# Performance work log

Measured on AMD Instinct MI355X. Metric: run time of the kernel, lower is better.

## Reference

```python
import jax, jax.numpy as jnp
import numpy as np

B, T, ENC_H, DEC_H, ATTN = 128, 2048, 512, 512, 128


def setup_inputs() -> dict:
    key = jax.random.key(0)
    k1, k2, k3, k4, k5 = jax.random.split(key, 5)
    s = lambda fan_in: 1.0 / np.sqrt(fan_in)
    return {
        "encoder_outputs": jax.random.normal(k1, (B, T, ENC_H), dtype=jnp.float32),
        "decoder_hidden": jax.random.normal(k2, (B, DEC_H), dtype=jnp.float32),
        # nn.Linear weights are [out_features, in_features]
        "W_enc": jax.random.uniform(k3, (ATTN, ENC_H), jnp.float32, -s(ENC_H), s(ENC_H)),
        "W_dec": jax.random.uniform(k4, (ATTN, DEC_H), jnp.float32, -s(DEC_H), s(DEC_H)),
        "v_w": jax.random.uniform(k5, (1, ATTN), jnp.float32, -s(ATTN), s(ATTN)),
    }


def reference(encoder_outputs, decoder_hidden, W_enc, W_dec, v_w):
    # enc_proj: [B, T, A]
    enc_proj = jnp.einsum("bth,ah->bta", encoder_outputs, W_enc)
    # dec_proj: [B, 1, A]
    dec_proj = jnp.einsum("bh,ah->ba", decoder_hidden, W_dec)[:, None, :]
    energy = jnp.tanh(enc_proj + dec_proj)                      # [B, T, A]
    scores = jnp.einsum("bta,a->bt", energy, v_w[0])            # [B, T]
    weights = jax.nn.softmax(scores, axis=-1)                   # [B, T]
    context = jnp.einsum("bt,bth->bh", weights, encoder_outputs)  # [B, ENC_H]
    return context, weights
```

## Files before the change

kernel.cpp:

```cpp
#include <hip/hip_runtime.h>
#include <hip/hip_bf16.h>

#define B_SZ   128
#define T_SZ   2048
#define ENCH   512
#define ATTN_  128
#define NBLK   256
#define SEGS_PER_BLK 4

typedef __attribute__((ext_vector_type(8))) short short8;
typedef __attribute__((ext_vector_type(4))) float f32x4;

__device__ __forceinline__ unsigned short f2bf_rne(float f) {
  unsigned u = __builtin_bit_cast(unsigned, f);
  u += 0x7FFFu + ((u >> 16) & 1u);
  return (unsigned short)(u >> 16);
}
__device__ __forceinline__ float fast_tanh(float x) {
  float e = __expf(2.f * x);
  return 1.f - __fdividef(2.f, e + 1.f);
}
__device__ __forceinline__ short8 pack8(float4 a, float4 b) {
  union { unsigned u[4]; short8 s; } r;
  asm("v_cvt_pk_bf16_f32 %0, %1, %2" : "=v"(r.u[0]) : "v"(a.x), "v"(a.y));
  asm("v_cvt_pk_bf16_f32 %0, %1, %2" : "=v"(r.u[1]) : "v"(a.z), "v"(a.w));
  asm("v_cvt_pk_bf16_f32 %0, %1, %2" : "=v"(r.u[2]) : "v"(b.x), "v"(b.y));
  asm("v_cvt_pk_bf16_f32 %0, %1, %2" : "=v"(r.u[3]) : "v"(b.z), "v"(b.w));
  return r.s;
}
template<int CTRL>
__device__ __forceinline__ float dpp_add(float v) {
  int t = __builtin_amdgcn_update_dpp(0, __builtin_bit_cast(int, v),
                                      CTRL, 0xf, 0xf, true);
  return v + __builtin_bit_cast(float, t);
}
__device__ __forceinline__ float sum16(float v) {
  v = dpp_add<0xB1>(v);
  v = dpp_add<0x4E>(v);
  v = dpp_add<0x141>(v);
  v = dpp_add<0x140>(v);
  return v;
}
__device__ __forceinline__ float bfel(short8 v, int j_half, bool hi) {
  unsigned u = __builtin_bit_cast(unsigned, (int)((((int*)&v))[j_half]));
  return __builtin_bit_cast(float, hi ? (u & 0xFFFF0000u) : (u << 16));
}

__global__ void k_prep(const float* __restrict__ w,
                       unsigned short* __restrict__ o,
                       const float* __restrict__ dec,
                       const float* __restrict__ wdec,
                       float* __restrict__ dout) {
  if (blockIdx.x < 32) {
    int idx = blockIdx.x * 256 + threadIdx.x;
    int l   = idx & 63;
    int wks = idx >> 6;
    int cg  = wks >> 4, ks = wks & 15;
    int row = cg * 16 + (l & 15);
    int col = ks * 32 + (l >> 4) * 8;
    const float4* src = reinterpret_cast<const float4*>(w + row * ENCH + col);
    float4 v0 = src[0], v1 = src[1];
    short8 r;
    r[0] = (short)f2bf_rne(v0.x); r[1] = (short)f2bf_rne(v0.y);
    r[2] = (short)f2bf_rne(v0.z); r[3] = (short)f2bf_rne(v0.w);
    r[4] = (short)f2bf_rne(v1.x); r[5] = (short)f2bf_rne(v1.y);
    r[6] = (short)f2bf_rne(v1.z); r[7] = (short)f2bf_rne(v1.w);
    *reinterpret_cast<short8*>(o + (size_t)idx * 8) = r;
  } else {
    __shared__ float dh[ENCH];
    int b = blockIdx.x - 32, tid = threadIdx.x;
    for (int i = tid; i < ENCH; i += 256) dh[i] = dec[b * ENCH + i];
    __syncthreads();
    if (tid < 128) {
      const float4* wr4 = reinterpret_cast<const float4*>(wdec + tid * ENCH);
      float acc = 0.f;
      for (int h4 = 0; h4 < ENCH / 4; ++h4) {
        float4 w4 = wr4[h4];
        acc += dh[h4 * 4 + 0] * w4.x + dh[h4 * 4 + 1] * w4.y +
               dh[h4 * 4 + 2] * w4.z + dh[h4 * 4 + 3] * w4.w;
      }
      dout[b * ATTN_ + tid] = acc;
    }
  }
}

__global__ __launch_bounds__(1024, 4) void k_main(
    const float* __restrict__ enc,
    const unsigned short* __restrict__ wfrag,
    const float* __restrict__ decproj,
    const float* __restrict__ vw,
    float* __restrict__ scores_raw,
    float* __restrict__ ctx_part,
    float* __restrict__ ml_part)
{
  const int tid  = threadIdx.x;
  const int lane = tid & 63;
  const int wid  = tid >> 6;
  const int l15  = lane & 15;
  const int g    = lane >> 4;

  __shared__ unsigned short w_lds[ATTN_ * ENCH];
  __shared__ float dv_lds[ATTN_], vv_lds[ATTN_];

  const int b    = blockIdx.x >> 1;
  const int seg0 = (blockIdx.x & 1) * 4;

#pragma unroll
  for (int r = 0; r < 8; ++r) {
    int i = r * 1024 + tid;
    reinterpret_cast<short8*>(w_lds)[i] = reinterpret_cast<const short8*>(wfrag)[i];
  }
  if (tid < 128)       dv_lds[tid] = decproj[b * ATTN_ + tid];
  else if (tid < 256)  vv_lds[tid - 128] = vw[tid - 128];
  __syncthreads();

#pragma unroll 1
  for (int k = 0; k < wid; ++k) __builtin_amdgcn_s_sleep(6);

  float m_run = -INFINITY, l_run = 0.f;
  float ctx8[8];
#pragma unroll
  for (int j = 0; j < 8; ++j) ctx8[j] = 0.f;

#pragma unroll 1
  for (int i = 0; i < SEGS_PER_BLK; ++i) {
    const int seg  = seg0 + i;
    const int row0 = seg * 256 + wid * 16;
    const float* arow = enc + ((size_t)b * T_SZ + row0 + l15) * ENCH + g * 8;

    short8 af[16];
#pragma unroll
    for (int ks = 0; ks < 16; ++ks) {
      float4 a0 = *reinterpret_cast<const float4*>(arow + ks * 32);
      float4 a1 = *reinterpret_cast<const float4*>(arow + ks * 32 + 4);
      af[ks] = pack8(a0, a1);
    }

    float e[4] = {0.f, 0.f, 0.f, 0.f};
#pragma unroll 1
    for (int half = 0; half < 2; ++half) {
      f32x4 acc[4];
#pragma unroll
      for (int c = 0; c < 4; ++c) acc[c] = (f32x4){0.f, 0.f, 0.f, 0.f};
#pragma unroll
      for (int ks = 0; ks < 16; ++ks) {
        const char* wb = (const char*)w_lds + ks * 1024 + lane * 16 + half * 65536;
#pragma unroll
        for (int c = 0; c < 4; ++c) {
          short8 bf = *reinterpret_cast<const short8*>(wb + c * 16384);
          acc[c] = __builtin_amdgcn_mfma_f32_16x16x32_bf16(af[ks], bf, acc[c], 0, 0, 0);
        }
      }
#pragma unroll
      for (int c = 0; c < 4; ++c) {
        int col = (half * 4 + c) * 16 + l15;
        float d = dv_lds[col], v = vv_lds[col];
#pragma unroll
        for (int r = 0; r < 4; ++r)
          e[r] += fast_tanh(acc[c][r] + d) * v;
      }
    }

    float er[4];
#pragma unroll
    for (int r = 0; r < 4; ++r) er[r] = sum16(e[r]);
    if (l15 == 0) {
#pragma unroll
      for (int r = 0; r < 4; ++r)
        scores_raw[(size_t)b * T_SZ + row0 + g * 4 + r] = er[r];
    }

    float mg = fmaxf(fmaxf(er[0], er[1]), fmaxf(er[2], er[3]));
    mg = fmaxf(mg, __shfl_xor(mg, 16));
    mg = fmaxf(mg, __shfl_xor(mg, 32));
    float x0 = __expf(er[0] - mg), x1 = __expf(er[1] - mg);
    float x2 = __expf(er[2] - mg), x3 = __expf(er[3] - mg);
    float xs = (x0 + x1) + (x2 + x3);
    xs += __shfl_xor(xs, 16);
    xs += __shfl_xor(xs, 32);
    float sel = (l15 & 3) == 0 ? er[0]
              : (l15 & 3) == 1 ? er[1]
              : (l15 & 3) == 2 ? er[2] : er[3];
    float smine = __shfl(sel, ((l15 >> 2) << 4) | (l15 & 3));
    const float p_me = __expf(smine - mg);

    float cseg[8];
#pragma unroll
    for (int j = 0; j < 8; ++j) cseg[j] = 0.f;
#pragma unroll
    for (int ks = 0; ks < 16; ++ks) {
      float c[8];
#pragma unroll
      for (int jh = 0; jh < 4; ++jh) {
        c[jh * 2 + 0] = p_me * bfel(af[ks], jh, false);
        c[jh * 2 + 1] = p_me * bfel(af[ks], jh, true);
      }
#pragma unroll
      for (int j = 0; j < 8; ++j) c[j] = sum16(c[j]);
      if (l15 == ks) {
#pragma unroll
        for (int j = 0; j < 8; ++j) cseg[j] = c[j];
      }
    }

    float m_new  = fmaxf(m_run, mg);
    float scale  = __expf(m_run - m_new);
    float fseg   = __expf(mg - m_new);
    l_run = l_run * scale + xs * fseg;
#pragma unroll
    for (int j = 0; j < 8; ++j) ctx8[j] = ctx8[j] * scale + cseg[j] * fseg;
    m_run = m_new;
  }

  __syncthreads();
  float* cred = reinterpret_cast<float*>(w_lds);
  float* cp = cred + wid * ENCH + l15 * 32 + g * 8;
#pragma unroll
  for (int j = 0; j < 8; ++j) cp[j] = ctx8[j];
  if (lane == 0) { dv_lds[wid * 2] = m_run; dv_lds[wid * 2 + 1] = l_run; }
  __syncthreads();

  if (tid < ENCH) {
    float M = dv_lds[0];
#pragma unroll
    for (int w = 1; w < 16; ++w) M = fmaxf(M, dv_lds[w * 2]);
    float L = 0.f, c = 0.f;
#pragma unroll
    for (int w = 0; w < 16; ++w) {
      float f = __expf(dv_lds[w * 2] - M);
      L += f * dv_lds[w * 2 + 1];
      c += f * cred[w * ENCH + tid];
    }
    const int widx2 = b * 2 + (blockIdx.x & 1);
    ctx_part[(size_t)widx2 * ENCH + tid] = c;
    if (tid == 0) {
      ml_part[widx2 * 2 + 0] = M;
      ml_part[widx2 * 2 + 1] = L;
    }
  }
}

__global__ void k_combine(const float* __restrict__ ctx_part,
                          const float* __restrict__ ml_part,
                          float* __restrict__ out_ctx,
                          float* __restrict__ weights)
{
  __shared__ float f0s, f1s, Msh, Lsh;
  int b = blockIdx.x, tid = threadIdx.x;
  if (tid == 0) {
    float m0 = ml_part[b * 4 + 0], l0 = ml_part[b * 4 + 1];
    float m1 = ml_part[b * 4 + 2], l1 = ml_part[b * 4 + 3];
    float M  = fmaxf(m0, m1);
    float f0 = __expf(m0 - M), f1 = __expf(m1 - M);
    Msh = M; Lsh = f0 * l0 + f1 * l1; f0s = f0; f1s = f1;
  }
  __syncthreads();
  float M = Msh, Linv = 1.f / Lsh, f0 = f0s, f1 = f1s;
  for (int h = tid; h < ENCH; h += 256) {
    float a = f0 * ctx_part[(size_t)(b * 2) * ENCH + h] +
              f1 * ctx_part[(size_t)(b * 2 + 1) * ENCH + h];
    out_ctx[b * ENCH + h] = a * Linv;
  }
  for (int t = tid; t < T_SZ; t += 256) {
    float raw = weights[(size_t)b * T_SZ + t];
    weights[(size_t)b * T_SZ + t] = __expf(raw - M) * Linv;
  }
}

extern "C" void kernel_launch(void* const* d_in, const int* in_sizes, int n_in,
                              void* d_out, int out_size, void* d_ws, size_t ws_size,
                              hipStream_t stream) {
  const float* enc  = (const float*)d_in[0];
  const float* dec  = (const float*)d_in[1];
  const float* wenc = (const float*)d_in[2];
  const float* wdec = (const float*)d_in[3];
  const float* vw   = (const float*)d_in[4];

  float* out     = (float*)d_out;
  float* out_ctx = out;
  float* out_w   = out + B_SZ * ENCH;

  char* ws = (char*)d_ws;
  unsigned short* wfrag = (unsigned short*)ws;
  float* decproj  = (float*)(ws + 131072);
  float* ml_part  = (float*)(ws + 131072 + 65536);
  float* ctx_part = (float*)(ws + 131072 + 65536 + 2048);

  hipLaunchKernelGGL(k_prep, dim3(160), dim3(256), 0, stream,
                     wenc, wfrag, dec, wdec, decproj);
  hipLaunchKernelGGL(k_main, dim3(NBLK), dim3(1024), 0, stream,
                     enc, wfrag, decproj, vw, out_w, ctx_part, ml_part);
  hipLaunchKernelGGL(k_combine, dim3(B_SZ), dim3(256), 0, stream,
                     ctx_part, ml_part, out_ctx, out_w);
}
```

Baseline: 148.4 us.

## Software-pipeline encoder row loads with MFMA compute across segments

Global loads of the encoder tile are split into four chunks that are interleaved with the first-half MFMAs, and the first chunk of the next segment is prefetched during the second half. The half loop is unrolled by hand so this staging can be expressed. The goal is to hide global-memory latency behind matrix math instead of loading all 16 fragments up front. It adds live registers for the prefetch buffers, which may lower occupancy.

Result: slower. 172.5 us (+16.3%).

```diff
diff --git a/kernel.cpp b/kernel.cpp
--- a/kernel.cpp
+++ b/kernel.cpp
@@ -122,29 +122,75 @@
 #pragma unroll
   for (int j = 0; j < 8; ++j) ctx8[j] = 0.f;
 
+  const float* arow = enc + ((size_t)b * T_SZ + seg0 * 256 + wid * 16 + l15) * ENCH + g * 8;
+
+  float4 ta[4], tb[4];
+#pragma unroll
+  for (int j = 0; j < 4; ++j) {
+    ta[j] = *reinterpret_cast<const float4*>(arow + j * 32);
+    tb[j] = *reinterpret_cast<const float4*>(arow + j * 32 + 4);
+  }
+
 #pragma unroll 1
   for (int i = 0; i < SEGS_PER_BLK; ++i) {
     const int seg  = seg0 + i;
     const int row0 = seg * 256 + wid * 16;
-    const float* arow = enc + ((size_t)b * T_SZ + row0 + l15) * ENCH + g * 8;
 
     short8 af[16];
-#pragma unroll
-    for (int ks = 0; ks < 16; ++ks) {
-      float4 a0 = *reinterpret_cast<const float4*>(arow + ks * 32);
-      float4 a1 = *reinterpret_cast<const float4*>(arow + ks * 32 + 4);
-      af[ks] = pack8(a0, a1);
-    }
-
     float e[4] = {0.f, 0.f, 0.f, 0.f};
-#pragma unroll 1
-    for (int half = 0; half < 2; ++half) {
+
+    {
       f32x4 acc[4];
 #pragma unroll
       for (int c = 0; c < 4; ++c) acc[c] = (f32x4){0.f, 0.f, 0.f, 0.f};
 #pragma unroll
+      for (int q = 0; q < 4; ++q) {
+#pragma unroll
+        for (int j = 0; j < 4; ++j) af[q * 4 + j] = pack8(ta[j], tb[j]);
+        if (q < 3) {
+#pragma unroll
+          for (int j = 0; j < 4; ++j) {
+            ta[j] = *reinterpret_cast<const float4*>(arow + (q * 4 + 4 + j) * 32);
+            tb[j] = *reinterpret_cast<const float4*>(arow + (q * 4 + 4 + j) * 32 + 4);
+          }
+        }
+#pragma unroll
+        for (int j = 0; j < 4; ++j) {
+          const int ks = q * 4 + j;
+          const char* wb = (const char*)w_lds + ks * 1024 + lane * 16;
+#pragma unroll
+          for (int c = 0; c < 4; ++c) {
+            short8 bf = *reinterpret_cast<const short8*>(wb + c * 16384);
+            acc[c] = __builtin_amdgcn_mfma_f32_16x16x32_bf16(af[ks], bf, acc[c], 0, 0, 0);
+          }
+        }
+      }
+#pragma unroll
+      for (int c = 0; c < 4; ++c) {
+        int col = c * 16 + l15;
+        float d = dv_lds[col], v = vv_lds[col];
+#pragma unroll
+        for (int r = 0; r < 4; ++r)
+          e[r] += fast_tanh(acc[c][r] + d) * v;
+      }
+    }
+
+    if (i + 1 < SEGS_PER_BLK) {
+      const float* anext = arow + 256 * ENCH;
+#pragma unroll
+      for (int j = 0; j < 4; ++j) {
+        ta[j] = *reinterpret_cast<const float4*>(anext + j * 32);
+        tb[j] = *reinterpret_cast<const float4*>(anext + j * 32 + 4);
+      }
+    }
+
+    {
+      f32x4 acc[4];
+#pragma unroll
+      for (int c = 0; c < 4; ++c) acc[c] = (f32x4){0.f, 0.f, 0.f, 0.f};
+#pragma unroll
       for (int ks = 0; ks < 16; ++ks) {
-        const char* wb = (const char*)w_lds + ks * 1024 + lane * 16 + half * 65536;
+        const char* wb = (const char*)w_lds + ks * 1024 + lane * 16 + 65536;
 #pragma unroll
         for (int c = 0; c < 4; ++c) {
           short8 bf = *reinterpret_cast<const short8*>(wb + c * 16384);
@@ -153,7 +199,7 @@
       }
 #pragma unroll
       for (int c = 0; c < 4; ++c) {
-        int col = (half * 4 + c) * 16 + l15;
+        int col = (4 + c) * 16 + l15;
         float d = dv_lds[col], v = vv_lds[col];
 #pragma unroll
         for (int r = 0; r < 4; ++r)
@@ -210,6 +256,8 @@
 #pragma unroll
     for (int j = 0; j < 8; ++j) ctx8[j] = ctx8[j] * scale + cseg[j] * fseg;
     m_run = m_new;
+
+    arow += 256 * ENCH;
   }
 
   __syncthreads();
```
